# Performance work log

Measured on AMD Instinct MI355X. Metric: run time of the kernel, lower is better.

Reference implementation:

```python
import jax, jax.numpy as jnp
import numpy as np

B, T, C = 2, 2048, 1024
NH, HD, DHR, L = 16, 64, 32, 512


def _rope(x, dim):
    # interleaved-pair RoPE; positions start at 1 (freq = arange(T)+1 in source)
    b, t, c = x.shape
    freq = jnp.arange(t, dtype=jnp.float32)[:, None] + 1.0
    pos = jnp.repeat(jnp.arange(dim // 2, dtype=jnp.float32), 2)[None, :]
    theta = jnp.exp(-2.0 * pos / dim * jnp.log(10000.0))
    cos, sin = jnp.cos(freq * theta), jnp.sin(freq * theta)
    xp = x.reshape(b, t, dim // 2, 2)
    xrot = jnp.stack([-xp[..., 1], xp[..., 0]], axis=-1).reshape(b, t, dim)
    return x * cos + xrot * sin


def _rms(x, g, eps=1e-6):
    return x * jax.lax.rsqrt(jnp.mean(x * x, axis=-1, keepdims=True) + eps) * g


def setup_inputs():
    key = jax.random.key(0)
    ks = jax.random.split(key, 10)
    w = lambda k, s: jax.random.normal(k, s, jnp.float32) * 0.02
    return {
        "x": jax.random.normal(ks[0], (B, T, C), jnp.float32),
        "w1": w(ks[1], (C, 2 * L)), "b1": jnp.zeros((2 * L,), jnp.float32),
        "wkr": w(ks[2], (2 * L, DHR)), "bkr": jnp.zeros((DHR,), jnp.float32),
        "wqr": w(ks[3], (2 * L, NH * DHR)), "bqr": jnp.zeros((NH * DHR,), jnp.float32),
        "wkv": w(ks[4], (L, 2 * C)), "bkv": jnp.zeros((2 * C,), jnp.float32),
        "wq": w(ks[5], (L, C)), "bq": jnp.zeros((C,), jnp.float32),
        "wo": w(ks[6], (C, C)), "bo": jnp.zeros((C,), jnp.float32),
        "wi": w(ks[7], (C, 4 * C)), "bi": jnp.zeros((4 * C,), jnp.float32),
        "wo2": w(ks[8], (4 * C, C)), "bo2": jnp.zeros((C,), jnp.float32),
        "g1": jnp.ones((C,), jnp.float32), "g2": jnp.ones((C,), jnp.float32),
    }


def reference(x, w1, b1, wkr, bkr, wqr, bqr, wkv, bkv, wq, bq, wo, bo,
              wi, bi, wo2, bo2, g1, g2):
    # ---- pre-norm MLA attention ----
    xn = _rms(x, g1)
    h = xn @ w1 + b1                                  # [B,T,2L]
    kv_lat, q_lat = jnp.split(h, 2, axis=-1)          # [B,T,L] each
    kr = _rope(h @ wkr + bkr, DHR)                    # [B,T,dhR] (input is the 2L concat, as in source)
    qr = _rope(h @ wqr + bqr, NH * DHR)               # RoPE over the full nh*dhR dim before head split
    qr = qr.reshape(B, T, NH, DHR).transpose(0, 2, 1, 3)   # [B,nh,T,dhR]
    k, v = jnp.split(kv_lat @ wkv + bkv, 2, axis=-1)  # [B,T,C] each
    q = q_lat @ wq + bq
    q, k, v = (a.reshape(B, T, NH, HD).transpose(0, 2, 1, 3) for a in (q, k, v))
    q = jnp.concatenate([q, qr], axis=-1)                                   # [B,nh,T,hd+dhR]
    k = jnp.concatenate([k, jnp.broadcast_to(kr[:, None], (B, NH, T, DHR))], axis=-1)
    dk = HD + DHR
    scores = jnp.einsum('bnsd,bntd->bnst', q, k) * dk ** -0.5               # fp32 logits
    mask = jnp.tril(jnp.ones((T, T), dtype=bool))
    scores = jnp.where(mask, scores, -jnp.inf)
    attn = jax.nn.softmax(scores, axis=-1)
    out = jnp.einsum('bnst,bntd->bnsd', attn, v)
    out = out.transpose(0, 2, 1, 3).reshape(B, T, C)
    x = x + out @ wo + bo
    # ---- pre-norm dense FFN ----
    xn2 = _rms(x, g2)
    ff = jax.nn.gelu(xn2 @ wi + bi) @ wo2 + bo2       # flax nn.gelu = tanh approx (jax default)
    return x + ff
```

## Files before the change

kernel.cpp:

```cpp
#include <hip/hip_runtime.h>
#include <math.h>


typedef __attribute__((ext_vector_type(8))) __bf16 bf16x8;
typedef __attribute__((ext_vector_type(4))) float f32x4;

__device__ __forceinline__ __bf16 bfbits(unsigned int u) {
    return __builtin_bit_cast(__bf16, (unsigned short)u);
}
__device__ __forceinline__ unsigned int packsplit(float x) {
    const __bf16 h = (__bf16)x;
    const __bf16 l = (__bf16)(x - (float)h);
    return (unsigned int)__builtin_bit_cast(unsigned short, h)
         | ((unsigned int)__builtin_bit_cast(unsigned short, l) << 16);
}
__device__ __forceinline__ float unpackf(unsigned int u) {
    const float hi = __builtin_bit_cast(float, u << 16);
    const float lo = __builtin_bit_cast(float, u & 0xffff0000u);
    return hi + lo;
}

__global__ __launch_bounds__(256) void split_pack_kernel(
    const float* __restrict__ w, unsigned int* __restrict__ wp, int n4)
{
    int i = blockIdx.x * 256 + threadIdx.x;
    const int stride = gridDim.x * 256;
    for (; i < n4; i += stride) {
        const float4 v = ((const float4*)w)[i];
        uint4 o;
        o.x = packsplit(v.x); o.y = packsplit(v.y);
        o.z = packsplit(v.z); o.w = packsplit(v.w);
        ((uint4*)wp)[i] = o;
    }
}

__global__ __launch_bounds__(256) void rmsnorm_kernel(
    const float* __restrict__ x, const float* __restrict__ g,
    unsigned int* __restrict__ outp)
{
    __shared__ float sm[4];
    const int row = blockIdx.x;
    const int tid = threadIdx.x;
    float4 v = ((const float4*)(x + (size_t)row * 1024))[tid];
    float ss = v.x * v.x + v.y * v.y + v.z * v.z + v.w * v.w;
    #pragma unroll
    for (int m = 32; m; m >>= 1) ss += __shfl_xor(ss, m, 64);
    if ((tid & 63) == 0) sm[tid >> 6] = ss;
    __syncthreads();
    const float total = sm[0] + sm[1] + sm[2] + sm[3];
    const float rstd = rsqrtf(total * (1.0f / 1024.0f) + 1e-6f);
    float4 gv = ((const float4*)g)[tid];
    uint4 o;
    o.x = packsplit(v.x * rstd * gv.x);
    o.y = packsplit(v.y * rstd * gv.y);
    o.z = packsplit(v.z * rstd * gv.z);
    o.w = packsplit(v.w * rstd * gv.w);
    ((uint4*)(outp + (size_t)row * 1024))[tid] = o;
}

__global__ __launch_bounds__(256, 2) void gemm_mfma_kernel(
    const unsigned int* __restrict__ Ap, int lda,
    const unsigned int* __restrict__ Wp,
    const float* __restrict__ bias,
    const float* __restrict__ res, int ldres,
    float* __restrict__ Cf,
    unsigned int* __restrict__ Cp, int ldc,
    int N, int K, int act)
{
    __shared__ __bf16 Ah[128 * 64];
    __shared__ __bf16 Al[128 * 64];
    __shared__ __bf16 Bh[128 * 64];
    __shared__ __bf16 Bl[128 * 64];

    const int tid = threadIdx.x;
    const int m0 = blockIdx.y * 128;
    const int n0 = blockIdx.x * 128;
    const int lane = tid & 63;
    const int w = tid >> 6;
    const int wm = (w >> 1) * 64;
    const int wn = (w & 1) * 64;

    f32x4 acc[4][4];
    #pragma unroll
    for (int i = 0; i < 4; ++i)
        #pragma unroll
        for (int j = 0; j < 4; ++j) acc[i][j] = (f32x4){0.f, 0.f, 0.f, 0.f};

    const int ar = tid >> 1;
    const int ak = (tid & 1) * 32;
    const int bc = tid & 127;
    const int bk = (tid >> 7) * 32;
    const int bcol = n0 + bc;
    const bool bok = bcol < N;

    for (int k0 = 0; k0 < K; k0 += 64) {
        __syncthreads();
        {
            const unsigned int* src = Ap + (size_t)(m0 + ar) * lda + k0 + ak;
            unsigned int ua[32];
            #pragma unroll
            for (int i = 0; i < 8; ++i) {
                uint4 v = ((const uint4*)src)[i];
                ua[i * 4 + 0] = v.x; ua[i * 4 + 1] = v.y;
                ua[i * 4 + 2] = v.z; ua[i * 4 + 3] = v.w;
            }
            #pragma unroll
            for (int s = 0; s < 4; ++s) {
                const int slot = (ak >> 3) + s;
                const int swz = slot ^ (ar & 7);
                bf16x8 hh, ll;
                #pragma unroll
                for (int j = 0; j < 8; ++j) {
                    const unsigned int p = ua[s * 8 + j];
                    hh[j] = bfbits(p);
                    ll[j] = bfbits(p >> 16);
                }
                *(bf16x8*)&Ah[ar * 64 + swz * 8] = hh;
                *(bf16x8*)&Al[ar * 64 + swz * 8] = ll;
            }
        }
        {
            const unsigned int* src = Wp + (size_t)(k0 + bk) * N + bcol;
            unsigned int up[32];
            #pragma unroll
            for (int j = 0; j < 32; ++j)
                up[j] = bok ? src[(size_t)j * N] : 0u;
            #pragma unroll
            for (int s = 0; s < 4; ++s) {
                const int slot = (bk >> 3) + s;
                const int swz = slot ^ (bc & 7);
                bf16x8 hh, ll;
                #pragma unroll
                for (int j = 0; j < 8; ++j) {
                    const unsigned int p = up[s * 8 + j];
                    hh[j] = bfbits(p);
                    ll[j] = bfbits(p >> 16);
                }
                *(bf16x8*)&Bh[bc * 64 + swz * 8] = hh;
                *(bf16x8*)&Bl[bc * 64 + swz * 8] = ll;
            }
        }
        __syncthreads();

        #pragma unroll
        for (int kc = 0; kc < 2; ++kc) {
            bf16x8 fAh[4], fAl[4], fBh[4], fBl[4];
            #pragma unroll
            for (int i = 0; i < 4; ++i) {
                const int row = wm + i * 16 + (lane & 15);
                const int slot = kc * 4 + (lane >> 4);
                const int offa = row * 64 + (slot ^ (row & 7)) * 8;
                fAh[i] = *(const bf16x8*)&Ah[offa];
                fAl[i] = *(const bf16x8*)&Al[offa];
                const int col = wn + i * 16 + (lane & 15);
                const int offb = col * 64 + (slot ^ (col & 7)) * 8;
                fBh[i] = *(const bf16x8*)&Bh[offb];
                fBl[i] = *(const bf16x8*)&Bl[offb];
            }
            #pragma unroll
            for (int i = 0; i < 4; ++i)
                #pragma unroll
                for (int j = 0; j < 4; ++j) {
                    acc[i][j] = __builtin_amdgcn_mfma_f32_16x16x32_bf16(
                        fAl[i], fBh[j], acc[i][j], 0, 0, 0);
                    acc[i][j] = __builtin_amdgcn_mfma_f32_16x16x32_bf16(
                        fAh[i], fBl[j], acc[i][j], 0, 0, 0);
                    acc[i][j] = __builtin_amdgcn_mfma_f32_16x16x32_bf16(
                        fAh[i], fBh[j], acc[i][j], 0, 0, 0);
                }
        }
    }

    const int rb = (lane >> 4) * 4;
    const int cc = lane & 15;
    #pragma unroll
    for (int j = 0; j < 4; ++j) {
        const int col = n0 + wn + j * 16 + cc;
        if (col >= N) continue;
        const float bv = bias[col];
        #pragma unroll
        for (int i = 0; i < 4; ++i) {
            #pragma unroll
            for (int r = 0; r < 4; ++r) {
                const int row = m0 + wm + i * 16 + rb + r;
                float v = acc[i][j][r] + bv;
                if (act == 1) {
                    const float t = 0.7978845608028654f * (v + 0.044715f * v * v * v);
                    v = 0.5f * v * (1.0f + tanhf(t));
                }
                if (res) v += res[(size_t)row * ldres + col];
                if (Cf) Cf[(size_t)row * ldc + col] = v;
                if (Cp) Cp[(size_t)row * ldc + col] = packsplit(v);
            }
        }
    }
}

__global__ void rope_kernel(unsigned int* __restrict__ buf, int dim, int npairs)
{
    const int idx = blockIdx.x * blockDim.x + threadIdx.x;
    if (idx >= npairs) return;
    const int hp = dim >> 1;
    const int row = idx / hp;
    const int p = idx - row * hp;
    const int t = row & 2047;
    const float theta = expf((float)p * (-2.0f / (float)dim) * 9.210340371976184f);
    const float pf = (float)(t + 1) * theta;
    double ang = fmod((double)pf, 6.283185307179586476925286766559);
    const float c = (float)cos(ang);
    const float s = (float)sin(ang);
    unsigned int* pr = buf + (size_t)row * dim + 2 * p;
    const float x0 = unpackf(pr[0]), x1 = unpackf(pr[1]);
    pr[0] = packsplit(x0 * c - x1 * s);
    pr[1] = packsplit(x1 * c + x0 * s);
}

#define KS  104
#define VTS 40
#define PSTR 40
__global__ __launch_bounds__(256) void attn_mfma_kernel(
    const unsigned int* __restrict__ q,
    const unsigned int* __restrict__ qr,
    const unsigned int* __restrict__ kv,
    const unsigned int* __restrict__ kr,
    unsigned int* __restrict__ att)
{
    __shared__ __bf16 Kh[32 * KS];
    __shared__ __bf16 Kl[32 * KS];
    __shared__ __bf16 Vth[64 * VTS];
    __shared__ __bf16 P[64 * PSTR];
    __shared__ float rsA[64], lsA[64];

    const int h = blockIdx.y, b = blockIdx.z;
    const int tid = threadIdx.x;
    const int lane = tid & 63;
    const int w = tid >> 6;
    const int lg = lane >> 4;
    const int l15 = lane & 15;
    const int rowK0 = b * 2048;
    const float scale = 0.10206207261596575f;

    #pragma unroll
    for (int ph = 0; ph < 2; ++ph) {
        const int qt = ph ? (31 - (int)blockIdx.x) : (int)blockIdx.x;
        const int rowQ0 = b * 2048 + qt * 64;
        const int qg = qt * 64 + w * 16 + l15;

        bf16x8 fQh[3], fQl[3];
        {
            const int grow = rowQ0 + w * 16 + l15;
            #pragma unroll
            for (int kc = 0; kc < 3; ++kc) {
                const unsigned int* src = (kc < 2)
                    ? q + (size_t)grow * 1024 + h * 64 + kc * 32 + lg * 8
                    : qr + (size_t)grow * 512 + h * 32 + lg * 8;
                #pragma unroll
                for (int j = 0; j < 8; ++j) {
                    const unsigned int u = src[j];
                    fQh[kc][j] = bfbits(u);
                    fQl[kc][j] = bfbits(u >> 16);
                }
            }
        }

        f32x4 accO[4];
        #pragma unroll
        for (int jd = 0; jd < 4; ++jd) accO[jd] = (f32x4){0.f, 0.f, 0.f, 0.f};
        float mold = -1e30f, lsum = 0.f;

        const int ntiles = 2 * qt + 2;
        for (int kt = 0; kt < ntiles; ++kt) {
            __syncthreads();
            #pragma unroll
            for (int i = 0; i < 8; ++i) {
                const int idx = tid + i * 256;
                const int r = idx >> 6, c = idx & 63;
                const unsigned int u =
                    kv[(size_t)(rowK0 + kt * 32 + r) * 2048 + h * 64 + c];
                Kh[r * KS + c] = bfbits(u);
                Kl[r * KS + c] = bfbits(u >> 16);
            }
            #pragma unroll
            for (int i = 0; i < 4; ++i) {
                const int idx = tid + i * 256;
                const int r = idx >> 5, c = idx & 31;
                const unsigned int u =
                    kr[(size_t)(rowK0 + kt * 32 + r) * 32 + c];
                Kh[r * KS + 64 + c] = bfbits(u);
                Kl[r * KS + 64 + c] = bfbits(u >> 16);
            }
            #pragma unroll
            for (int i = 0; i < 8; ++i) {
                const int idx = tid + i * 256;
                const int r = idx >> 6, c = idx & 63;
                const unsigned int u =
                    kv[(size_t)(rowK0 + kt * 32 + r) * 2048 + 1024 + h * 64 + c];
                Vth[c * VTS + r] = bfbits(u);
            }
            __syncthreads();

            f32x4 accS[2];
            accS[0] = (f32x4){0.f, 0.f, 0.f, 0.f};
            accS[1] = (f32x4){0.f, 0.f, 0.f, 0.f};
            #pragma unroll
            for (int jt = 0; jt < 2; ++jt) {
                #pragma unroll
                for (int kc = 0; kc < 3; ++kc) {
                    const int off = (jt * 16 + l15) * KS + kc * 32 + lg * 8;
                    const bf16x8 fKh = *(const bf16x8*)&Kh[off];
                    const bf16x8 fKl = *(const bf16x8*)&Kl[off];
                    accS[jt] = __builtin_amdgcn_mfma_f32_16x16x32_bf16(
                        fKl, fQh[kc], accS[jt], 0, 0, 0);
                    accS[jt] = __builtin_amdgcn_mfma_f32_16x16x32_bf16(
                        fKh, fQl[kc], accS[jt], 0, 0, 0);
                    accS[jt] = __builtin_amdgcn_mfma_f32_16x16x32_bf16(
                        fKh, fQh[kc], accS[jt], 0, 0, 0);
                }
            }

            float sv[2][4];
            #pragma unroll
            for (int jt = 0; jt < 2; ++jt)
                #pragma unroll
                for (int r = 0; r < 4; ++r) sv[jt][r] = accS[jt][r] * scale;
            if (kt * 32 + 31 > qt * 64 + w * 16) {
                #pragma unroll
                for (int jt = 0; jt < 2; ++jt)
                    #pragma unroll
                    for (int r = 0; r < 4; ++r) {
                        const int kvg = kt * 32 + jt * 16 + lg * 4 + r;
                        if (kvg > qg) sv[jt][r] = -1e30f;
                    }
            }

            float m8 = sv[0][0];
            #pragma unroll
            for (int jt = 0; jt < 2; ++jt)
                #pragma unroll
                for (int r = 0; r < 4; ++r) m8 = fmaxf(m8, sv[jt][r]);
            m8 = fmaxf(m8, __shfl_xor(m8, 16, 64));
            m8 = fmaxf(m8, __shfl_xor(m8, 32, 64));
            const float mnew = fmaxf(mold, m8);
            const float rs = expf(mold - mnew);
            float psum = 0.f;
            float pv[2][4];
            #pragma unroll
            for (int jt = 0; jt < 2; ++jt)
                #pragma unroll
                for (int r = 0; r < 4; ++r) {
                    const float p = expf(sv[jt][r] - mnew);
                    pv[jt][r] = p;
                    psum += p;
                }
            psum += __shfl_xor(psum, 16, 64);
            psum += __shfl_xor(psum, 32, 64);
            lsum = lsum * rs + psum;
            mold = mnew;

            #pragma unroll
            for (int jt = 0; jt < 2; ++jt)
                #pragma unroll
                for (int r = 0; r < 4; ++r)
                    P[(w * 16 + l15) * PSTR + jt * 16 + lg * 4 + r] =
                        (__bf16)pv[jt][r];
            if (lane < 16) rsA[w * 16 + lane] = rs;
            const f32x4 rsv = *(const f32x4*)&rsA[w * 16 + lg * 4];

            #pragma unroll
            for (int jd = 0; jd < 4; ++jd)
                #pragma unroll
                for (int r = 0; r < 4; ++r) accO[jd][r] *= rsv[r];

            const bf16x8 fP = *(const bf16x8*)&P[(w * 16 + l15) * PSTR + lg * 8];
            #pragma unroll
            for (int jd = 0; jd < 4; ++jd) {
                const bf16x8 fV = *(const bf16x8*)&Vth[(jd * 16 + l15) * VTS + lg * 8];
                accO[jd] = __builtin_amdgcn_mfma_f32_16x16x32_bf16(
                    fP, fV, accO[jd], 0, 0, 0);
            }
        }

        if (lane < 16) lsA[w * 16 + lane] = lsum;
        const f32x4 lsv = *(const f32x4*)&lsA[w * 16 + lg * 4];
        #pragma unroll
        for (int r = 0; r < 4; ++r) {
            const float linv = 1.0f / lsv[r];
            const int grow = rowQ0 + w * 16 + lg * 4 + r;
            #pragma unroll
            for (int jd = 0; jd < 4; ++jd)
                att[(size_t)grow * 1024 + h * 64 + jd * 16 + l15] =
                    packsplit(accO[jd][r] * linv);
        }
    }
}

static inline void gemm(hipStream_t s, const unsigned int* Ap, int lda,
                        const unsigned int* Wp,
                        const float* bias, const float* res, int ldres,
                        float* Cf, unsigned int* Cp, int ldc,
                        int M, int N, int K, int act)
{
    dim3 grid((N + 127) / 128, M / 128);
    gemm_mfma_kernel<<<grid, 256, 0, s>>>(Ap, lda, Wp, bias, res, ldres,
                                          Cf, Cp, ldc, N, K, act);
}

static inline void split_pack(hipStream_t s, const float* w, unsigned int* wp, int n)
{
    const int n4 = n >> 2;
    const int blocks = (n4 + 255) / 256 < 2048 ? (n4 + 255) / 256 : 2048;
    split_pack_kernel<<<blocks, 256, 0, s>>>(w, wp, n4);
}

extern "C" void kernel_launch(void* const* d_in, const int* in_sizes, int n_in,
                              void* d_out, int out_size, void* d_ws, size_t ws_size,
                              hipStream_t stream)
{
    const float* x   = (const float*)d_in[0];
    const float* w1  = (const float*)d_in[1];
    const float* b1  = (const float*)d_in[2];
    const float* wkr = (const float*)d_in[3];
    const float* bkr = (const float*)d_in[4];
    const float* wqr = (const float*)d_in[5];
    const float* bqr = (const float*)d_in[6];
    const float* wkv = (const float*)d_in[7];
    const float* bkv = (const float*)d_in[8];
    const float* wq  = (const float*)d_in[9];
    const float* bq  = (const float*)d_in[10];
    const float* wo  = (const float*)d_in[11];
    const float* bo  = (const float*)d_in[12];
    const float* wi  = (const float*)d_in[13];
    const float* bi  = (const float*)d_in[14];
    const float* wo2 = (const float*)d_in[15];
    const float* bo2 = (const float*)d_in[16];
    const float* g1  = (const float*)d_in[17];
    const float* g2  = (const float*)d_in[18];
    float* out = (float*)d_out;
    float* ws  = (float*)d_ws;

    const size_t MF = (size_t)1 << 20;
    unsigned int* xnp  = (unsigned int*)ws;
    unsigned int* hbp  = (unsigned int*)(ws + 4 * MF);
    unsigned int* kvbp = (unsigned int*)(ws + 8 * MF);
    unsigned int* qbp  = (unsigned int*)(ws + 16 * MF);
    unsigned int* qrbp = (unsigned int*)(ws + 20 * MF);
    unsigned int* krbp = (unsigned int*)(ws + 22 * MF);
    unsigned int* attbp = hbp;
    unsigned int* ffhp  = hbp;
    unsigned int* w1p  = (unsigned int*)(ws + 23 * MF);
    unsigned int* wkrp = (unsigned int*)(ws + 24 * MF);
    unsigned int* wqrp = (unsigned int*)(ws + 25 * MF);
    unsigned int* wkvp = (unsigned int*)(ws + 26 * MF);
    unsigned int* wqp  = (unsigned int*)(ws + 27 * MF);
    unsigned int* wop  = (unsigned int*)(ws + 28 * MF);
    unsigned int* wip  = (unsigned int*)(ws + 29 * MF);
    unsigned int* wo2p = (unsigned int*)(ws + 33 * MF);

    split_pack(stream, w1,  w1p,  1024 * 1024);
    split_pack(stream, wkr, wkrp, 1024 * 32);
    split_pack(stream, wqr, wqrp, 1024 * 512);
    split_pack(stream, wkv, wkvp, 512 * 2048);
    split_pack(stream, wq,  wqp,  512 * 1024);
    split_pack(stream, wo,  wop,  1024 * 1024);
    split_pack(stream, wi,  wip,  1024 * 4096);
    split_pack(stream, wo2, wo2p, 4096 * 1024);

    rmsnorm_kernel<<<4096, 256, 0, stream>>>(x, g1, xnp);
    gemm(stream, xnp, 1024, w1p, b1, nullptr, 0, nullptr, hbp, 1024,
         4096, 1024, 1024, 0);
    gemm(stream, hbp, 1024, wkrp, bkr, nullptr, 0, nullptr, krbp, 32,
         4096, 32, 1024, 0);
    gemm(stream, hbp, 1024, wqrp, bqr, nullptr, 0, nullptr, qrbp, 512,
         4096, 512, 1024, 0);
    gemm(stream, hbp, 1024, wkvp, bkv, nullptr, 0, nullptr, kvbp, 2048,
         4096, 2048, 512, 0);
    gemm(stream, hbp + 512, 1024, wqp, bq, nullptr, 0, nullptr, qbp, 1024,
         4096, 1024, 512, 0);
    rope_kernel<<<(4096 * 16 + 255) / 256, 256, 0, stream>>>(krbp, 32, 4096 * 16);
    rope_kernel<<<(4096 * 256 + 255) / 256, 256, 0, stream>>>(qrbp, 512, 4096 * 256);
    attn_mfma_kernel<<<dim3(16, 16, 2), 256, 0, stream>>>(qbp, qrbp, kvbp, krbp, attbp);
    gemm(stream, attbp, 1024, wop, bo, x, 1024, out, nullptr, 1024,
         4096, 1024, 1024, 0);

    rmsnorm_kernel<<<4096, 256, 0, stream>>>(out, g2, xnp);
    gemm(stream, xnp, 1024, wip, bi, nullptr, 0, nullptr, ffhp, 4096,
         4096, 4096, 1024, 1);
    gemm(stream, ffhp, 4096, wo2p, bo2, out, 1024, out, nullptr, 1024,
         4096, 1024, 4096, 0);
}
```

Measured before the change: 969.7 us.

## Pre-transpose weights and double-buffer GEMM tiles via direct global-to-LDS loads

Result: faster. 867.7 us (-10.5%).

```diff
diff --git a/kernel.cpp b/kernel.cpp
--- a/kernel.cpp
+++ b/kernel.cpp
@@ -20,18 +20,28 @@
     return hi + lo;
 }
 
-__global__ __launch_bounds__(256) void split_pack_kernel(
-    const float* __restrict__ w, unsigned int* __restrict__ wp, int n4)
-{
-    int i = blockIdx.x * 256 + threadIdx.x;
-    const int stride = gridDim.x * 256;
-    for (; i < n4; i += stride) {
-        const float4 v = ((const float4*)w)[i];
-        uint4 o;
-        o.x = packsplit(v.x); o.y = packsplit(v.y);
-        o.z = packsplit(v.z); o.w = packsplit(v.w);
-        ((uint4*)wp)[i] = o;
-    }
+__device__ __forceinline__ void gl_lds16(const unsigned int* g, unsigned int* l) {
+    __builtin_amdgcn_global_load_lds(
+        (const __attribute__((address_space(1))) unsigned int*)g,
+        (__attribute__((address_space(3))) unsigned int*)l,
+        16, 0, 0);
+}
+
+__global__ __launch_bounds__(256) void transpose_pack_kernel(
+    const float* __restrict__ w, unsigned int* __restrict__ wt,
+    int N, int K)
+{
+    __shared__ float t[32][33];
+    const int k0 = blockIdx.x * 32, n0 = blockIdx.y * 32;
+    const int tx = threadIdx.x & 31, ty = threadIdx.x >> 5;
+    #pragma unroll
+    for (int r = 0; r < 4; ++r)
+        t[ty + r * 8][tx] = w[(size_t)(k0 + ty + r * 8) * N + n0 + tx];
+    __syncthreads();
+    #pragma unroll
+    for (int r = 0; r < 4; ++r)
+        wt[(size_t)(n0 + ty + r * 8) * K + k0 + tx] =
+            packsplit(t[tx][ty + r * 8]);
 }
 
 __global__ __launch_bounds__(256) void rmsnorm_kernel(
@@ -60,17 +70,14 @@
 
 __global__ __launch_bounds__(256, 2) void gemm_mfma_kernel(
     const unsigned int* __restrict__ Ap, int lda,
-    const unsigned int* __restrict__ Wp,
+    const unsigned int* __restrict__ Bt, int ldb,
     const float* __restrict__ bias,
     const float* __restrict__ res, int ldres,
     float* __restrict__ Cf,
     unsigned int* __restrict__ Cp, int ldc,
     int N, int K, int act)
 {
-    __shared__ __bf16 Ah[128 * 64];
-    __shared__ __bf16 Al[128 * 64];
-    __shared__ __bf16 Bh[128 * 64];
-    __shared__ __bf16 Bl[128 * 64];
+    __shared__ unsigned int lds[2][8192];
 
     const int tid = threadIdx.x;
     const int m0 = blockIdx.y * 128;
@@ -79,6 +86,19 @@
     const int w = tid >> 6;
     const int wm = (w >> 1) * 64;
     const int wn = (w & 1) * 64;
+    const int l15 = lane & 15;
+    const int lg = lane >> 4;
+
+    const int srow = lane >> 3;
+    const int sslot = lane & 7;
+    const unsigned int* asrc[4];
+    const unsigned int* bsrc[4];
+    #pragma unroll
+    for (int i = 0; i < 4; ++i) {
+        const int row = w * 32 + i * 8 + srow;
+        asrc[i] = Ap + (size_t)(m0 + row) * lda + (sslot ^ (row & 7)) * 4;
+        bsrc[i] = Bt + (size_t)(n0 + row) * ldb + (sslot ^ (row & 7)) * 4;
+    }
 
     f32x4 acc[4][4];
     #pragma unroll
@@ -86,89 +106,80 @@
         #pragma unroll
         for (int j = 0; j < 4; ++j) acc[i][j] = (f32x4){0.f, 0.f, 0.f, 0.f};
 
-    const int ar = tid >> 1;
-    const int ak = (tid & 1) * 32;
-    const int bc = tid & 127;
-    const int bk = (tid >> 7) * 32;
-    const int bcol = n0 + bc;
-    const bool bok = bcol < N;
-
-    for (int k0 = 0; k0 < K; k0 += 64) {
+    const int nt = K >> 5;
+
+    #pragma unroll
+    for (int i = 0; i < 4; ++i) {
+        gl_lds16(asrc[i], &lds[0][w * 1024 + i * 256]);
+        gl_lds16(bsrc[i], &lds[0][4096 + w * 1024 + i * 256]);
+    }
+    __syncthreads();
+
+    for (int t = 0; t < nt; ++t) {
+        const int cur = t & 1;
+        if (t + 1 < nt) {
+            const int k1 = (t + 1) << 5;
+            #pragma unroll
+            for (int i = 0; i < 4; ++i) {
+                gl_lds16(asrc[i] + k1, &lds[cur ^ 1][w * 1024 + i * 256]);
+                gl_lds16(bsrc[i] + k1, &lds[cur ^ 1][4096 + w * 1024 + i * 256]);
+            }
+        }
+
+        bf16x8 fAh[4], fAl[4], fBh[4], fBl[4];
+        #pragma unroll
+        for (int i = 0; i < 4; ++i) {
+            {
+                const int row = wm + i * 16 + l15;
+                const int s0 = (lg * 2) ^ (row & 7);
+                const int s1 = (lg * 2 + 1) ^ (row & 7);
+                const uint4 p0 = *(const uint4*)&lds[cur][row * 32 + s0 * 4];
+                const uint4 p1 = *(const uint4*)&lds[cur][row * 32 + s1 * 4];
+                uint4 h, l;
+                h.x = __builtin_amdgcn_perm(p0.y, p0.x, 0x05040100u);
+                l.x = __builtin_amdgcn_perm(p0.y, p0.x, 0x07060302u);
+                h.y = __builtin_amdgcn_perm(p0.w, p0.z, 0x05040100u);
+                l.y = __builtin_amdgcn_perm(p0.w, p0.z, 0x07060302u);
+                h.z = __builtin_amdgcn_perm(p1.y, p1.x, 0x05040100u);
+                l.z = __builtin_amdgcn_perm(p1.y, p1.x, 0x07060302u);
+                h.w = __builtin_amdgcn_perm(p1.w, p1.z, 0x05040100u);
+                l.w = __builtin_amdgcn_perm(p1.w, p1.z, 0x07060302u);
+                fAh[i] = __builtin_bit_cast(bf16x8, h);
+                fAl[i] = __builtin_bit_cast(bf16x8, l);
+            }
+            {
+                const int row = wn + i * 16 + l15;
+                const int s0 = (lg * 2) ^ (row & 7);
+                const int s1 = (lg * 2 + 1) ^ (row & 7);
+                const uint4 p0 = *(const uint4*)&lds[cur][4096 + row * 32 + s0 * 4];
+                const uint4 p1 = *(const uint4*)&lds[cur][4096 + row * 32 + s1 * 4];
+                uint4 h, l;
+                h.x = __builtin_amdgcn_perm(p0.y, p0.x, 0x05040100u);
+                l.x = __builtin_amdgcn_perm(p0.y, p0.x, 0x07060302u);
+                h.y = __builtin_amdgcn_perm(p0.w, p0.z, 0x05040100u);
+                l.y = __builtin_amdgcn_perm(p0.w, p0.z, 0x07060302u);
+                h.z = __builtin_amdgcn_perm(p1.y, p1.x, 0x05040100u);
+                l.z = __builtin_amdgcn_perm(p1.y, p1.x, 0x07060302u);
+                h.w = __builtin_amdgcn_perm(p1.w, p1.z, 0x05040100u);
+                l.w = __builtin_amdgcn_perm(p1.w, p1.z, 0x07060302u);
+                fBh[i] = __builtin_bit_cast(bf16x8, h);
+                fBl[i] = __builtin_bit_cast(bf16x8, l);
+            }
+        }
+
+        #pragma unroll
+        for (int i = 0; i < 4; ++i)
+            #pragma unroll
+            for (int j = 0; j < 4; ++j) {
+                acc[i][j] = __builtin_amdgcn_mfma_f32_16x16x32_bf16(
+                    fAl[i], fBh[j], acc[i][j], 0, 0, 0);
+                acc[i][j] = __builtin_amdgcn_mfma_f32_16x16x32_bf16(
+                    fAh[i], fBl[j], acc[i][j], 0, 0, 0);
+                acc[i][j] = __builtin_amdgcn_mfma_f32_16x16x32_bf16(
+                    fAh[i], fBh[j], acc[i][j], 0, 0, 0);
+            }
+
         __syncthreads();
-        {
-            const unsigned int* src = Ap + (size_t)(m0 + ar) * lda + k0 + ak;
-            unsigned int ua[32];
-            #pragma unroll
-            for (int i = 0; i < 8; ++i) {
-                uint4 v = ((const uint4*)src)[i];
-                ua[i * 4 + 0] = v.x; ua[i * 4 + 1] = v.y;
-                ua[i * 4 + 2] = v.z; ua[i * 4 + 3] = v.w;
-            }
-            #pragma unroll
-            for (int s = 0; s < 4; ++s) {
-                const int slot = (ak >> 3) + s;
-                const int swz = slot ^ (ar & 7);
-                bf16x8 hh, ll;
-                #pragma unroll
-                for (int j = 0; j < 8; ++j) {
-                    const unsigned int p = ua[s * 8 + j];
-                    hh[j] = bfbits(p);
-                    ll[j] = bfbits(p >> 16);
-                }
-                *(bf16x8*)&Ah[ar * 64 + swz * 8] = hh;
-                *(bf16x8*)&Al[ar * 64 + swz * 8] = ll;
-            }
-        }
-        {
-            const unsigned int* src = Wp + (size_t)(k0 + bk) * N + bcol;
-            unsigned int up[32];
-            #pragma unroll
-            for (int j = 0; j < 32; ++j)
-                up[j] = bok ? src[(size_t)j * N] : 0u;
-            #pragma unroll
-            for (int s = 0; s < 4; ++s) {
-                const int slot = (bk >> 3) + s;
-                const int swz = slot ^ (bc & 7);
-                bf16x8 hh, ll;
-                #pragma unroll
-                for (int j = 0; j < 8; ++j) {
-                    const unsigned int p = up[s * 8 + j];
-                    hh[j] = bfbits(p);
-                    ll[j] = bfbits(p >> 16);
-                }
-                *(bf16x8*)&Bh[bc * 64 + swz * 8] = hh;
-                *(bf16x8*)&Bl[bc * 64 + swz * 8] = ll;
-            }
-        }
-        __syncthreads();
-
-        #pragma unroll
-        for (int kc = 0; kc < 2; ++kc) {
-            bf16x8 fAh[4], fAl[4], fBh[4], fBl[4];
-            #pragma unroll
-            for (int i = 0; i < 4; ++i) {
-                const int row = wm + i * 16 + (lane & 15);
-                const int slot = kc * 4 + (lane >> 4);
-                const int offa = row * 64 + (slot ^ (row & 7)) * 8;
-                fAh[i] = *(const bf16x8*)&Ah[offa];
-                fAl[i] = *(const bf16x8*)&Al[offa];
-                const int col = wn + i * 16 + (lane & 15);
-                const int offb = col * 64 + (slot ^ (col & 7)) * 8;
-                fBh[i] = *(const bf16x8*)&Bh[offb];
-                fBl[i] = *(const bf16x8*)&Bl[offb];
-            }
-            #pragma unroll
-            for (int i = 0; i < 4; ++i)
-                #pragma unroll
-                for (int j = 0; j < 4; ++j) {
-                    acc[i][j] = __builtin_amdgcn_mfma_f32_16x16x32_bf16(
-                        fAl[i], fBh[j], acc[i][j], 0, 0, 0);
-                    acc[i][j] = __builtin_amdgcn_mfma_f32_16x16x32_bf16(
-                        fAh[i], fBl[j], acc[i][j], 0, 0, 0);
-                    acc[i][j] = __builtin_amdgcn_mfma_f32_16x16x32_bf16(
-                        fAh[i], fBh[j], acc[i][j], 0, 0, 0);
-                }
-        }
     }
 
     const int rb = (lane >> 4) * 4;
@@ -395,21 +406,21 @@
 }
 
 static inline void gemm(hipStream_t s, const unsigned int* Ap, int lda,
-                        const unsigned int* Wp,
+                        const unsigned int* Bt, int ldb,
                         const float* bias, const float* res, int ldres,
                         float* Cf, unsigned int* Cp, int ldc,
                         int M, int N, int K, int act)
 {
     dim3 grid((N + 127) / 128, M / 128);
-    gemm_mfma_kernel<<<grid, 256, 0, s>>>(Ap, lda, Wp, bias, res, ldres,
+    gemm_mfma_kernel<<<grid, 256, 0, s>>>(Ap, lda, Bt, ldb, bias, res, ldres,
                                           Cf, Cp, ldc, N, K, act);
 }
 
-static inline void split_pack(hipStream_t s, const float* w, unsigned int* wp, int n)
-{
-    const int n4 = n >> 2;
-    const int blocks = (n4 + 255) / 256 < 2048 ? (n4 + 255) / 256 : 2048;
-    split_pack_kernel<<<blocks, 256, 0, s>>>(w, wp, n4);
+static inline void tpack(hipStream_t s, const float* w, unsigned int* wt,
+                         int K, int N)
+{
+    dim3 grid(K / 32, N / 32);
+    transpose_pack_kernel<<<grid, 256, 0, s>>>(w, wt, N, K);
 }
 
 extern "C" void kernel_launch(void* const* d_in, const int* in_sizes, int n_in,
@@ -447,44 +458,44 @@
     unsigned int* krbp = (unsigned int*)(ws + 22 * MF);
     unsigned int* attbp = hbp;
     unsigned int* ffhp  = hbp;
-    unsigned int* w1p  = (unsigned int*)(ws + 23 * MF);
-    unsigned int* wkrp = (unsigned int*)(ws + 24 * MF);
-    unsigned int* wqrp = (unsigned int*)(ws + 25 * MF);
-    unsigned int* wkvp = (unsigned int*)(ws + 26 * MF);
-    unsigned int* wqp  = (unsigned int*)(ws + 27 * MF);
-    unsigned int* wop  = (unsigned int*)(ws + 28 * MF);
-    unsigned int* wip  = (unsigned int*)(ws + 29 * MF);
-    unsigned int* wo2p = (unsigned int*)(ws + 33 * MF);
-
-    split_pack(stream, w1,  w1p,  1024 * 1024);
-    split_pack(stream, wkr, wkrp, 1024 * 32);
-    split_pack(stream, wqr, wqrp, 1024 * 512);
-    split_pack(stream, wkv, wkvp, 512 * 2048);
-    split_pack(stream, wq,  wqp,  512 * 1024);
-    split_pack(stream, wo,  wop,  1024 * 1024);
-    split_pack(stream, wi,  wip,  1024 * 4096);
-    split_pack(stream, wo2, wo2p, 4096 * 1024);
+    unsigned int* w1T  = (unsigned int*)(ws + 23 * MF);
+    unsigned int* wkrT = (unsigned int*)(ws + 24 * MF);
+    unsigned int* wqrT = (unsigned int*)(ws + 25 * MF);
+    unsigned int* wkvT = (unsigned int*)(ws + 26 * MF);
+    unsigned int* wqT  = (unsigned int*)(ws + 27 * MF);
+    unsigned int* woT  = (unsigned int*)(ws + 28 * MF);
+    unsigned int* wiT  = (unsigned int*)(ws + 29 * MF);
+    unsigned int* wo2T = (unsigned int*)(ws + 33 * MF);
+
+    tpack(stream, w1,  w1T,  1024, 1024);
+    tpack(stream, wkr, wkrT, 1024, 32);
+    tpack(stream, wqr, wqrT, 1024, 512);
+    tpack(stream, wkv, wkvT, 512, 2048);
+    tpack(stream, wq,  wqT,  512, 1024);
+    tpack(stream, wo,  woT,  1024, 1024);
+    tpack(stream, wi,  wiT,  1024, 4096);
+    tpack(stream, wo2, wo2T, 4096, 1024);
 
     rmsnorm_kernel<<<4096, 256, 0, stream>>>(x, g1, xnp);
-    gemm(stream, xnp, 1024, w1p, b1, nullptr, 0, nullptr, hbp, 1024,
+    gemm(stream, xnp, 1024, w1T, 1024, b1, nullptr, 0, nullptr, hbp, 1024,
          4096, 1024, 1024, 0);
-    gemm(stream, hbp, 1024, wkrp, bkr, nullptr, 0, nullptr, krbp, 32,
+    gemm(stream, hbp, 1024, wkrT, 1024, bkr, nullptr, 0, nullptr, krbp, 32,
          4096, 32, 1024, 0);
-    gemm(stream, hbp, 1024, wqrp, bqr, nullptr, 0, nullptr, qrbp, 512,
+    gemm(stream, hbp, 1024, wqrT, 1024, bqr, nullptr, 0, nullptr, qrbp, 512,
          4096, 512, 1024, 0);
-    gemm(stream, hbp, 1024, wkvp, bkv, nullptr, 0, nullptr, kvbp, 2048,
+    gemm(stream, hbp, 1024, wkvT, 512, bkv, nullptr, 0, nullptr, kvbp, 2048,
          4096, 2048, 512, 0);
-    gemm(stream, hbp + 512, 1024, wqp, bq, nullptr, 0, nullptr, qbp, 1024,
+    gemm(stream, hbp + 512, 1024, wqT, 512, bq, nullptr, 0, nullptr, qbp, 1024,
          4096, 1024, 512, 0);
     rope_kernel<<<(4096 * 16 + 255) / 256, 256, 0, stream>>>(krbp, 32, 4096 * 16);
     rope_kernel<<<(4096 * 256 + 255) / 256, 256, 0, stream>>>(qrbp, 512, 4096 * 256);
     attn_mfma_kernel<<<dim3(16, 16, 2), 256, 0, stream>>>(qbp, qrbp, kvbp, krbp, attbp);
-    gemm(stream, attbp, 1024, wop, bo, x, 1024, out, nullptr, 1024,
+    gemm(stream, attbp, 1024, woT, 1024, bo, x, 1024, out, nullptr, 1024,
          4096, 1024, 1024, 0);
 
     rmsnorm_kernel<<<4096, 256, 0, stream>>>(out, g2, xnp);
-    gemm(stream, xnp, 1024, wip, bi, nullptr, 0, nullptr, ffhp, 4096,
+    gemm(stream, xnp, 1024, wiT, 1024, bi, nullptr, 0, nullptr, ffhp, 4096,
          4096, 4096, 1024, 1);
-    gemm(stream, ffhp, 4096, wo2p, bo2, out, 1024, out, nullptr, 1024,
+    gemm(stream, ffhp, 4096, wo2T, 4096, bo2, out, 1024, out, nullptr, 1024,
          4096, 1024, 4096, 0);
 }
```
